# Kernel tuning notes

Measured on AMD Instinct MI355X. Metric: run time of the kernel, lower is better.

The kernel has to match this reference:

```python
import jax, jax.numpy as jnp
import numpy as np

DECAY = 0.999
EPS = 1e-05
COMMIT = 0.25


def _layer_norm(x, g, b, eps=1e-5):
    mu = x.mean(-1, keepdims=True)
    var = ((x - mu) ** 2).mean(-1, keepdims=True)
    return (x - mu) * jax.lax.rsqrt(var + eps) * g + b


def setup_inputs() -> dict:
    key = jax.random.key(0)
    ks = jax.random.split(key, 8)
    B, T, D, M, H = 8, 4096, 512, 1024, 512
    init_bound = 1.0 / 512
    embedding = jax.random.uniform(ks[0], (M, D), jnp.float32, -init_bound, init_bound)
    return {
        "dense_x": jax.random.normal(ks[1], (B, T, D), jnp.float32),
        "dense_padding_mask": jax.random.randint(ks[2], (B, T), 0, 2).astype(bool),
        "labels": jax.random.randint(ks[3], (B, T), 0, M),
        "embedding": embedding,
        "ema_count": jnp.zeros((M,), jnp.float32),
        "ema_weight": embedding,
        "ln1_g": jnp.ones((D,), jnp.float32),
        "ln1_b": jnp.zeros((D,), jnp.float32),
        "W1": jax.random.normal(ks[4], (D, H), jnp.float32) * (1.0 / np.sqrt(D)),
        "ln2_g": jnp.ones((H,), jnp.float32),
        "ln2_b": jnp.zeros((H,), jnp.float32),
        "W2": jax.random.normal(ks[5], (H, M), jnp.float32) * (1.0 / np.sqrt(H)),
    }


def reference(dense_x, dense_padding_mask, labels, embedding, ema_count, ema_weight,
              ln1_g, ln1_b, W1, ln2_g, ln2_b, W2):
    B, T, D = dense_x.shape
    M = embedding.shape[0]
    N = B * T

    # ---- VQ codebook (EMA) ----
    x_flat = jax.lax.stop_gradient(dense_x).reshape(N, D)
    distances = (jnp.sum(embedding ** 2, axis=1)[None, :]
                 + jnp.sum(x_flat ** 2, axis=1, keepdims=True)
                 - 2.0 * (x_flat @ embedding.T))
    indices = jnp.argmin(distances, axis=-1)  # [N]
    quantized = embedding[indices].reshape(B, T, D)

    # EMA codebook update (training path); encodings.sum(0) and encodings.T @ x
    # expressed as scatter-adds instead of materializing [N, M] one-hot.
    counts = jnp.zeros((M,), dense_x.dtype).at[indices].add(1.0)
    new_count = DECAY * ema_count + (1.0 - DECAY) * counts
    n = jnp.sum(new_count)
    new_count = (new_count + EPS) / (n + M * EPS) * n
    dw = jnp.zeros((M, D), dense_x.dtype).at[indices].add(x_flat)
    new_weight = DECAY * ema_weight + (1.0 - DECAY) * dw
    new_embedding = new_weight / new_count[:, None]

    e_latent_loss = (dense_x - jax.lax.stop_gradient(quantized)) ** 2  # [B,T,D]
    vq_loss = COMMIT * e_latent_loss
    quantized_st = dense_x + jax.lax.stop_gradient(quantized - dense_x)

    avg_probs = counts / N
    perplexity = jnp.exp(-jnp.sum(avg_probs * jnp.log(avg_probs + 1e-10)))

    # ---- decoder: LN -> ReLU -> Linear -> LN -> ReLU -> Linear ----
    h = jax.nn.relu(_layer_norm(dense_x, ln1_g, ln1_b)) @ W1      # [B,T,H]
    logits = jax.nn.relu(_layer_norm(h, ln2_g, ln2_b)) @ W2       # [B,T,M]

    # ---- cross-entropy with ignore_index=-1 (padding) ----
    lab = jnp.where(dense_padding_mask, -1, labels)
    valid = lab >= 0
    safe = jnp.where(valid, lab, 0)
    logp = jax.nn.log_softmax(logits, axis=-1)
    ce = -jnp.take_along_axis(logp, safe[..., None], axis=-1)[..., 0]
    recon_loss = jnp.where(valid, ce, 0.0)

    loss = recon_loss + vq_loss.sum(-1)  # [B,T]
    return quantized_st, loss, perplexity, new_embedding, new_count, new_weight
```

## Files before the change

### kernel.cpp

```cpp
#include <hip/hip_runtime.h>


#define N_TOK 32768
#define WAITV(n) __builtin_amdgcn_s_waitcnt(0x0F70 | (n))
#define BAR() __builtin_amdgcn_s_barrier()

typedef __attribute__((ext_vector_type(8))) short short8;
typedef _Float16 half8 __attribute__((ext_vector_type(8)));
typedef __attribute__((ext_vector_type(4))) float f32x4;

__device__ __forceinline__ f32x4 mfma16(short8 a, short8 b, f32x4 c) {
    return __builtin_amdgcn_mfma_f32_16x16x32_bf16(a, b, c, 0, 0, 0);
}
__device__ __forceinline__ f32x4 mfma16h(half8 a, half8 b, f32x4 c) {
    return __builtin_amdgcn_mfma_f32_16x16x32_f16(a, b, c, 0, 0, 0);
}

__device__ __forceinline__ void gl_lds16(const unsigned short* g, char* l) {
    __builtin_amdgcn_global_load_lds(
        (const __attribute__((address_space(1))) void*)g,
        (__attribute__((address_space(3))) void*)l, 16, 0, 0);
}

__device__ __forceinline__ unsigned short f2bf(float x) {
    unsigned u = __float_as_uint(x);
    u += 0x7fffu + ((u >> 16) & 1u);
    return (unsigned short)(u >> 16);
}
__device__ __forceinline__ float bf2f(unsigned short h) {
    return __uint_as_float(((unsigned)h) << 16);
}
__device__ __forceinline__ unsigned short f2h(float x) {
    union { _Float16 h; unsigned short u; } c;
    c.h = (_Float16)x;
    return c.u;
}
__device__ __forceinline__ float h2f(unsigned short u) {
    union { _Float16 h; unsigned short u; } c;
    c.u = u;
    return (float)c.h;
}

__device__ __forceinline__ float waveSum(float v) {
#pragma unroll
    for (int off = 32; off > 0; off >>= 1) v += __shfl_down(v, off, 64);
    return v;
}
__device__ __forceinline__ float xorSum(float v) {
#pragma unroll
    for (int off = 1; off < 64; off <<= 1) v += __shfl_xor(v, off);
    return v;
}

__global__ __launch_bounds__(256) void prep_x_kernel(
        const float* __restrict__ X, const float* __restrict__ g,
        const float* __restrict__ b, unsigned short* __restrict__ Xf,
        unsigned short* __restrict__ A1, unsigned long long* __restrict__ minpack) {
    int tid = threadIdx.x;
    if (tid < 4) minpack[(blockIdx.x << 2) + tid] = ~0ULL;
    int lane = tid & 63;
    int n = (blockIdx.x << 2) + (tid >> 6);
    const float* row = X + ((size_t)n << 9);
    float v[8]; float s = 0.f, ss = 0.f;
#pragma unroll
    for (int i = 0; i < 8; ++i) { v[i] = row[lane + (i << 6)]; s += v[i]; ss += v[i] * v[i]; }
    s = xorSum(s); ss = xorSum(ss);
    float mu = s * (1.f / 512.f);
    float rs = rsqrtf(ss * (1.f / 512.f) - mu * mu + 1e-5f);
#pragma unroll
    for (int i = 0; i < 8; ++i) {
        int c = lane + (i << 6);
        size_t o = ((size_t)n << 9) + c;
        float x = v[i];
        Xf[o] = f2h(x);
        float a = fmaxf((x - mu) * rs * g[c] + b[c], 0.f);
        A1[o] = f2bf(a);
    }
}

__global__ __launch_bounds__(256) void prep_e_kernel(
        const float* __restrict__ E, unsigned short* __restrict__ Ehf,
        unsigned short* __restrict__ Elf, float* __restrict__ e_sq,
        int* __restrict__ izero) {
    if (blockIdx.x < 8) izero[(blockIdx.x << 8) + threadIdx.x] = 0;
    int lane = threadIdx.x & 63;
    int m = (blockIdx.x << 2) + (threadIdx.x >> 6);
    const float* row = E + ((size_t)m << 9);
    float ss = 0.f;
#pragma unroll
    for (int i = 0; i < 8; ++i) {
        int c = lane + (i << 6);
        float x = row[c];
        ss += x * x;
        float xs = x * 512.f;
        unsigned short h = f2h(xs);
        size_t o = ((size_t)m << 9) + c;
        Ehf[o] = h;
        Elf[o] = f2h(xs - h2f(h));
    }
    ss = xorSum(ss);
    if (lane == 0) e_sq[m] = ss * 512.f;
}

__global__ __launch_bounds__(256) void prep_wt_kernel(
        const float* __restrict__ W1, const float* __restrict__ W2,
        unsigned short* __restrict__ W1T, unsigned short* __restrict__ W2T) {
    __shared__ float t[32][33];
    int bx = blockIdx.x;
    const float* W = (bx < 16) ? W1 : W2;
    unsigned short* WT = (bx < 16) ? W1T : W2T;
    int Nw = (bx < 16) ? 512 : 1024;
    int n0 = ((bx < 16) ? bx : (bx - 16)) << 5, k0 = blockIdx.y << 5;
    int tx = threadIdx.x & 31, ty = threadIdx.x >> 5;
#pragma unroll
    for (int l = 0; l < 4; ++l)
        t[ty + (l << 3)][tx] = W[(size_t)(k0 + ty + (l << 3)) * Nw + n0 + tx];
    __syncthreads();
#pragma unroll
    for (int l = 0; l < 4; ++l)
        WT[(((size_t)(n0 + ty + (l << 3))) << 9) + k0 + tx] = f2bf(t[tx][ty + (l << 3)]);
}

__device__ __forceinline__ unsigned long long packDist(float d, int m) {
    unsigned u = __float_as_uint(d);
    u = (u & 0x80000000u) ? ~u : (u | 0x80000000u);
    return ((unsigned long long)u << 32) | (unsigned)m;
}

__device__ __forceinline__ void dist_body(
        int q, int x, char* LB,
        const unsigned short* __restrict__ Xf,
        const unsigned short* __restrict__ Ehf, const unsigned short* __restrict__ Elf,
        const float* __restrict__ e_sq, unsigned long long* __restrict__ minpack) {
    int tid = threadIdx.x, lane = tid & 63, w = tid >> 6;
    int quad = lane >> 4, lanelo = lane & 15;
    int wm = w >> 1, wn = w & 1;
    int row0 = (((q >> 3) << 3) | x) << 8;
    int m0 = (q & 7) << 7;

    int mA = tid & 255, kA = tid >> 8;
    int nB = tid & 127, kB = tid >> 7;
    const unsigned short* pA = Xf  + (((size_t)(row0 + mA)) << 9) + (kA << 3);
    const unsigned short* pH = Ehf + (((size_t)(m0  + nB)) << 9) + (kB << 3);
    const unsigned short* pL = Elf + (((size_t)(m0  + nB)) << 9) + (kB << 3);
    char* dA = LB + (tid << 4);
    char* dB = LB + 16384 + (tid << 4);
    const char* ra  = LB + (quad << 12) + (((wm << 6) + lanelo) << 4);
    const char* rbh = LB + 16384 + (quad << 11) + (((wn << 6) + lanelo) << 4);

    f32x4 acc[4][4];
#pragma unroll
    for (int i = 0; i < 4; ++i)
#pragma unroll
        for (int j = 0; j < 4; ++j) acc[i][j] = 0.f;

    gl_lds16(pA, dA);   gl_lds16(pA + 16, dA + 8192);
    gl_lds16(pH, dB);   gl_lds16(pL, dB + 8192);

#pragma unroll
    for (int it = 0; it < 16; ++it) {
        const int cb = it & 1;
        if (it < 15) {
            const unsigned short* sA = pA + ((it + 1) << 5);
            const unsigned short* sH = pH + ((it + 1) << 5);
            const unsigned short* sL = pL + ((it + 1) << 5);
            char* eA = dA + (cb ^ 1) * 32768;
            char* eB = dB + (cb ^ 1) * 32768;
            gl_lds16(sA, eA);   gl_lds16(sA + 16, eA + 8192);
            gl_lds16(sH, eB);   gl_lds16(sL, eB + 8192);
            WAITV(4);
        } else {
            WAITV(0);
        }
        BAR();
        const char* A  = ra  + cb * 32768;
        const char* Bh = rbh + cb * 32768;
        half8 av[4], bh[4], bl[4];
#pragma unroll
        for (int i = 0; i < 4; ++i) av[i] = *(const half8*)(A + (i << 8));
#pragma unroll
        for (int j = 0; j < 4; ++j) {
            bh[j] = *(const half8*)(Bh + (j << 8));
            bl[j] = *(const half8*)(Bh + 8192 + (j << 8));
        }
#pragma unroll
        for (int i = 0; i < 4; ++i)
#pragma unroll
            for (int j = 0; j < 4; ++j) acc[i][j] = mfma16h(av[i], bh[j], acc[i][j]);
#pragma unroll
        for (int i = 0; i < 4; ++i)
#pragma unroll
            for (int j = 0; j < 4; ++j) acc[i][j] = mfma16h(av[i], bl[j], acc[i][j]);
        BAR();
    }

    float esq[4];
#pragma unroll
    for (int j = 0; j < 4; ++j) esq[j] = e_sq[m0 + (wn << 6) + (j << 4) + lanelo];
#pragma unroll
    for (int i = 0; i < 4; ++i)
#pragma unroll
        for (int r = 0; r < 4; ++r) {
            unsigned long long best = ~0ULL;
#pragma unroll
            for (int j = 0; j < 4; ++j) {
                int code = m0 + (wn << 6) + (j << 4) + lanelo;
                float d = esq[j] - 2.f * acc[i][j][r];
                unsigned long long p = packDist(d, code);
                if (p < best) best = p;
            }
#pragma unroll
            for (int off = 1; off < 16; off <<= 1) {
                unsigned long long q2 = __shfl_xor(best, off);
                if (q2 < best) best = q2;
            }
            if (lanelo == 0) {
                int t = row0 + (wm << 6) + (i << 4) + (quad << 2) + r;
                atomicMin(&minpack[t], best);
            }
        }
}

__device__ __forceinline__ void gemm_core512(
        char* LB, const unsigned short* pA, const unsigned short* pB,
        f32x4 (*acc)[4]) {
    int tid = threadIdx.x, lane = tid & 63, w = tid >> 6;
    int quad = lane >> 4, lanelo = lane & 15;
    int wm = w >> 1, wn = w & 1;
    char* dA = LB + (tid << 4);
    char* dB = LB + 16384 + (tid << 4);
    const char* ra = LB + (quad << 12) + (((wm << 6) + lanelo) << 4);
    const char* rb = LB + 16384 + (quad << 11) + (((wn << 6) + lanelo) << 4);

    gl_lds16(pA, dA);   gl_lds16(pA + 16, dA + 8192);
    gl_lds16(pB, dB);

#pragma unroll
    for (int it = 0; it < 16; ++it) {
        const int cb = it & 1;
        if (it < 15) {
            const unsigned short* sA = pA + ((it + 1) << 5);
            const unsigned short* sB = pB + ((it + 1) << 5);
            char* eA = dA + (cb ^ 1) * 24576;
            char* eB = dB + (cb ^ 1) * 24576;
            gl_lds16(sA, eA);   gl_lds16(sA + 16, eA + 8192);
            gl_lds16(sB, eB);
            WAITV(3);
        } else {
            WAITV(0);
        }
        BAR();
        const char* A = ra + cb * 24576;
        const char* B = rb + cb * 24576;
        short8 af[4], bf4[4];
#pragma unroll
        for (int i = 0; i < 4; ++i) af[i] = *(const short8*)(A + (i << 8));
#pragma unroll
        for (int j = 0; j < 4; ++j) bf4[j] = *(const short8*)(B + (j << 8));
#pragma unroll
        for (int i = 0; i < 4; ++i)
#pragma unroll
            for (int j = 0; j < 4; ++j) acc[i][j] = mfma16(af[i], bf4[j], acc[i][j]);
        BAR();
    }
}

__device__ __forceinline__ void gemm1_body(
        int g, int x, char* LB,
        const unsigned short* __restrict__ A1, const unsigned short* __restrict__ W1T,
        unsigned short* __restrict__ Hb) {
    int tid = threadIdx.x, lane = tid & 63, w = tid >> 6;
    int quad = lane >> 4, lanelo = lane & 15;
    int wm = w >> 1, wn = w & 1;
    int row0 = (((g >> 2) << 3) | x) << 8;
    int n0 = (g & 3) << 7;

    int mA = tid & 255, kA = tid >> 8;
    int nB = tid & 127, kB = tid >> 7;
    const unsigned short* pA = A1  + (((size_t)(row0 + mA)) << 9) + (kA << 3);
    const unsigned short* pB = W1T + (((size_t)(n0   + nB)) << 9) + (kB << 3);

    f32x4 acc[4][4];
#pragma unroll
    for (int i = 0; i < 4; ++i)
#pragma unroll
        for (int j = 0; j < 4; ++j) acc[i][j] = 0.f;

    gemm_core512(LB, pA, pB, acc);

#pragma unroll
    for (int i = 0; i < 4; ++i)
#pragma unroll
        for (int j = 0; j < 4; ++j)
#pragma unroll
            for (int r = 0; r < 4; ++r) {
                int row = row0 + (wm << 6) + (i << 4) + (quad << 2) + r;
                int col = n0 + (wn << 6) + (j << 4) + lanelo;
                Hb[((size_t)row << 9) + col] = f2bf(acc[i][j][r]);
            }
}

__global__ __launch_bounds__(512) void fused1_kernel(
        const unsigned short* __restrict__ Xf,
        const unsigned short* __restrict__ Ehf, const unsigned short* __restrict__ Elf,
        const float* __restrict__ e_sq, unsigned long long* __restrict__ minpack,
        const unsigned short* __restrict__ A1, const unsigned short* __restrict__ W1T,
        unsigned short* __restrict__ Hb) {
    __shared__ __align__(16) char LB[65536];
    int b = blockIdx.x, x = b & 7, m = b >> 3;
    int t = m % 3, g = m / 3;
    if (t < 2) dist_body((g << 1) + t, x, LB, Xf, Ehf, Elf, e_sq, minpack);
    else       gemm1_body(g, x, LB, A1, W1T, Hb);
}

__global__ __launch_bounds__(256) void fused2_kernel(
        const float* __restrict__ X, const float* __restrict__ E,
        const unsigned long long* __restrict__ minpack,
        float* __restrict__ out_q, int* __restrict__ icounts,
        float* __restrict__ vqsum,
        const unsigned short* __restrict__ Hb, const float* __restrict__ g2,
        const float* __restrict__ b2, unsigned short* __restrict__ A2) {
    int nb = blockIdx.x >> 1;
    int lane = threadIdx.x & 63;
    int n = (nb << 2) + (threadIdx.x >> 6);
    if ((blockIdx.x & 1) == 0) {
        int idx = (int)(minpack[n] & 0xFFFFFFFFULL);
        if (lane == 0) atomicAdd(&icounts[idx], 1);
        const float* xr = X + ((size_t)n << 9);
        const float* er = E + ((size_t)idx << 9);
        float s = 0.f;
#pragma unroll
        for (int i = 0; i < 8; ++i) {
            int c = lane + (i << 6);
            float xv = xr[c], q = er[c];
            out_q[((size_t)n << 9) + c] = q;
            float dlt = xv - q;
            s += dlt * dlt;
        }
        s = waveSum(s);
        if (lane == 0) vqsum[n] = 0.25f * s;
    } else {
        const unsigned short* row = Hb + ((size_t)n << 9);
        float v[8]; float s = 0.f, ss = 0.f;
#pragma unroll
        for (int i = 0; i < 8; ++i) { v[i] = bf2f(row[lane + (i << 6)]); s += v[i]; ss += v[i] * v[i]; }
        s = xorSum(s); ss = xorSum(ss);
        float mu = s * (1.f / 512.f);
        float rs = rsqrtf(ss * (1.f / 512.f) - mu * mu + 1e-5f);
#pragma unroll
        for (int i = 0; i < 8; ++i) {
            int c = lane + (i << 6);
            float a = fmaxf((v[i] - mu) * rs * g2[c] + b2[c], 0.f);
            A2[((size_t)n << 9) + c] = f2bf(a);
        }
    }
}

__global__ __launch_bounds__(1024) void codebook_kernel(
        const float* __restrict__ ema_count, const int* __restrict__ icounts,
        float* __restrict__ out_perp, float* __restrict__ out_newcount,
        int* __restrict__ offsets) {
    __shared__ int sc[1024];
    __shared__ float red[16];
    int tid = threadIdx.x;
    int lane = tid & 63, wid = tid >> 6;
    int ic = icounts[tid];
    sc[tid] = ic;
    for (int off = 1; off < 1024; off <<= 1) {
        __syncthreads();
        int v = (tid >= off) ? sc[tid - off] : 0;
        __syncthreads();
        sc[tid] += v;
    }
    offsets[tid] = sc[tid] - ic;
    __syncthreads();

    float cnt = (float)ic;
    float raw = 0.999f * ema_count[tid] + 0.001f * cnt;
    float v = waveSum(raw);
    if (lane == 0) red[wid] = v;
    __syncthreads();
    float nsum = 0.f;
#pragma unroll
    for (int i = 0; i < 16; ++i) nsum += red[i];
    __syncthreads();
    float p = cnt * (1.f / 32768.f);
    float e = p * logf(p + 1e-10f);
    e = waveSum(e);
    if (lane == 0) red[wid] = e;
    __syncthreads();
    float ent = 0.f;
#pragma unroll
    for (int i = 0; i < 16; ++i) ent += red[i];
    float nc = (raw + 1e-5f) / (nsum + 1024.f * 1e-5f) * nsum;
    out_newcount[tid] = nc;
    if (tid == 0) out_perp[0] = expf(-ent);
}

__global__ __launch_bounds__(256) void scatter_kernel(
        const unsigned long long* __restrict__ minpack,
        const int* __restrict__ offsets, int* __restrict__ cursor,
        int* __restrict__ bucket) {
    int n = (blockIdx.x << 8) + threadIdx.x;
    int idx = (int)(minpack[n] & 0xFFFFFFFFULL);
    int pos = atomicAdd(&cursor[idx], 1);
    bucket[offsets[idx] + pos] = n;
}

__device__ __forceinline__ void dw_body(
        int m, char* LB, const float* __restrict__ X,
        const int* __restrict__ bucket, const int* __restrict__ icounts,
        const int* __restrict__ offsets, float* __restrict__ dw) {
    float* comb = (float*)LB;
    int tid = threadIdx.x, lane = tid & 63, w = tid >> 6;
    int cnt = icounts[m], base = offsets[m];
    float acc[8] = {};
    for (int i = w; i < cnt; i += 8) {
        int t = bucket[base + i];
        const float* xr = X + ((size_t)t << 9);
#pragma unroll
        for (int j = 0; j < 8; ++j) acc[j] += xr[lane + (j << 6)];
    }
#pragma unroll
    for (int j = 0; j < 8; ++j) comb[(w << 9) + lane + (j << 6)] = acc[j];
    __syncthreads();
    int c = tid;
    if (c < 512) {
        float s = 0.f;
#pragma unroll
        for (int p = 0; p < 8; ++p) s += comb[(p << 9) + c];
        dw[((size_t)m << 9) + c] = s;
    }
}

__device__ __forceinline__ void gemm2_body(
        int q, int x, char* LB,
        float (*lmax)[2][64], float (*lsum)[2][64], float* llab, int* slab,
        const unsigned short* __restrict__ A2, const unsigned short* __restrict__ W2T,
        const int* __restrict__ mask, const int* __restrict__ labels,
        float* __restrict__ ws_cmax, float* __restrict__ ws_csum,
        float* __restrict__ ws_lab) {
    int tid = threadIdx.x, lane = tid & 63, w = tid >> 6;
    int quad = lane >> 4, lanelo = lane & 15;
    int wm = w >> 1, wn = w & 1;
    int row0 = (((q >> 3) << 3) | x) << 8;
    int cy = q & 7;
    int c0 = cy << 7;
    if (tid < 256) {
        int mk = mask[row0 + tid];
        slab[tid] = mk ? 0 : labels[row0 + tid];
    }
    __syncthreads();

    int mA = tid & 255, kA = tid >> 8;
    int nB = tid & 127, kB = tid >> 7;
    const unsigned short* pA = A2  + (((size_t)(row0 + mA)) << 9) + (kA << 3);
    const unsigned short* pB = W2T + (((size_t)(c0   + nB)) << 9) + (kB << 3);

    f32x4 acc[4][4];
#pragma unroll
    for (int i = 0; i < 4; ++i)
#pragma unroll
        for (int j = 0; j < 4; ++j) acc[i][j] = 0.f;

    gemm_core512(LB, pA, pB, acc);

#pragma unroll
    for (int i = 0; i < 4; ++i)
#pragma unroll
        for (int j = 0; j < 4; ++j)
#pragma unroll
            for (int r = 0; r < 4; ++r) {
                int code = c0 + (wn << 6) + (j << 4) + lanelo;
                int tt = (wm << 6) + (i << 4) + (quad << 2) + r;
                if (code == slab[tt]) llab[tt] = acc[i][j][r];
            }
#pragma unroll
    for (int i = 0; i < 4; ++i)
#pragma unroll
        for (int r = 0; r < 4; ++r) {
            float mx = fmaxf(fmaxf(acc[i][0][r], acc[i][1][r]),
                             fmaxf(acc[i][2][r], acc[i][3][r]));
#pragma unroll
            for (int off = 1; off < 16; off <<= 1) mx = fmaxf(mx, __shfl_xor(mx, off));
            if (lanelo == 0) lmax[wm][wn][(i << 4) + (quad << 2) + r] = mx;
        }
    __syncthreads();
#pragma unroll
    for (int i = 0; i < 4; ++i)
#pragma unroll
        for (int r = 0; r < 4; ++r) {
            int tl = (i << 4) + (quad << 2) + r;
            float cm = fmaxf(lmax[wm][0][tl], lmax[wm][1][tl]);
            float s2 = expf(acc[i][0][r] - cm) + expf(acc[i][1][r] - cm) +
                       expf(acc[i][2][r] - cm) + expf(acc[i][3][r] - cm);
#pragma unroll
            for (int off = 1; off < 16; off <<= 1) s2 += __shfl_xor(s2, off);
            if (lanelo == 0) lsum[wm][wn][tl] = s2;
        }
    __syncthreads();
    if (tid < 256) {
        int wmi = tid >> 6, tl = tid & 63;
        int token = row0 + tid;
        float cm = fmaxf(lmax[wmi][0][tl], lmax[wmi][1][tl]);
        float cs = lsum[wmi][0][tl] + lsum[wmi][1][tl];
        size_t o = ((size_t)cy << 15) + token;
        ws_cmax[o] = cm;
        ws_csum[o] = cs;
        if ((slab[tid] >> 7) == cy) ws_lab[token] = llab[tid];
    }
}

__global__ __launch_bounds__(512) void fused3_kernel(
        const unsigned short* __restrict__ A2, const unsigned short* __restrict__ W2T,
        const int* __restrict__ mask, const int* __restrict__ labels,
        float* __restrict__ ws_cmax, float* __restrict__ ws_csum,
        float* __restrict__ ws_lab,
        const float* __restrict__ X, const int* __restrict__ bucket,
        const int* __restrict__ icounts, const int* __restrict__ offsets,
        float* __restrict__ dw) {
    __shared__ __align__(16) char LB[49152];
    __shared__ float lmax[4][2][64], lsum[4][2][64], llab[256];
    __shared__ int slab[256];
    int b = blockIdx.x, x = b & 7, m = b >> 3;
    int t = m & 1, g = m >> 1;
    if (t == 0) gemm2_body(g, x, LB, lmax, lsum, llab, slab,
                           A2, W2T, mask, labels, ws_cmax, ws_csum, ws_lab);
    else        dw_body((g << 3) | x, LB, X, bucket, icounts, offsets, dw);
}

__global__ __launch_bounds__(256) void epilogue_kernel(
        const float* __restrict__ ema_weight, const float* __restrict__ dw,
        const float* __restrict__ newcount, float* __restrict__ out_neww,
        float* __restrict__ out_newemb,
        const float* __restrict__ ws_cmax, const float* __restrict__ ws_csum,
        const float* __restrict__ ws_lab, const int* __restrict__ mask,
        const float* __restrict__ vqsum, float* __restrict__ loss_out) {
    int bx = blockIdx.x;
    if (bx < 2048) {
        int i = (bx << 8) + threadIdx.x;
        float nw = 0.999f * ema_weight[i] + 0.001f * dw[i];
        out_neww[i] = nw;
        out_newemb[i] = nw / newcount[i >> 9];
    } else {
        int n = ((bx - 2048) << 8) + threadIdx.x;
        float m[8], s[8];
#pragma unroll
        for (int c = 0; c < 8; ++c) {
            m[c] = ws_cmax[(c << 15) + n];
            s[c] = ws_csum[(c << 15) + n];
        }
        float gm = m[0];
#pragma unroll
        for (int c = 1; c < 8; ++c) gm = fmaxf(gm, m[c]);
        float se = 0.f;
#pragma unroll
        for (int c = 0; c < 8; ++c) se += s[c] * expf(m[c] - gm);
        float ce = -(ws_lab[n] - gm - logf(se));
        loss_out[n] = (mask[n] ? 0.f : ce) + vqsum[n];
    }
}

extern "C" void kernel_launch(void* const* d_in, const int* in_sizes, int n_in,
                              void* d_out, int out_size, void* d_ws, size_t ws_size,
                              hipStream_t stream) {
    const float* X          = (const float*)d_in[0];
    const int*   mask       = (const int*)d_in[1];
    const int*   labels     = (const int*)d_in[2];
    const float* E          = (const float*)d_in[3];
    const float* ema_count  = (const float*)d_in[4];
    const float* ema_weight = (const float*)d_in[5];
    const float* g1 = (const float*)d_in[6];
    const float* b1 = (const float*)d_in[7];
    const float* W1 = (const float*)d_in[8];
    const float* g2 = (const float*)d_in[9];
    const float* b2 = (const float*)d_in[10];
    const float* W2 = (const float*)d_in[11];

    float* out = (float*)d_out;
    float* out_q        = out;
    float* out_loss     = out + 16777216;
    float* out_perp     = out + 16809984;
    float* out_newemb   = out + 16809985;
    float* out_newcount = out + 17334273;
    float* out_neww     = out + 17335297;

    float* w = (float*)d_ws;
    float* vqsum = w;  w += 32768;
    float* e_sq = w;   w += 1024;
    float* dwbuf = w;  w += 524288;
    unsigned long long* minpack = (unsigned long long*)w; w += 65536;
    float* ws_cmax = w; w += 262144;
    float* ws_csum = w; w += 262144;
    float* ws_lab  = w; w += 32768;
    int* icounts = (int*)w; w += 1024;
    int* cursor  = (int*)w; w += 1024;
    int* offsets = (int*)w; w += 1024;
    int* bucket  = (int*)w; w += 32768;
    unsigned short* Ehf = (unsigned short*)w; w += 262144;
    unsigned short* Elf = (unsigned short*)w; w += 262144;
    unsigned short* W1T = (unsigned short*)w; w += 131072;
    unsigned short* W2T = (unsigned short*)w; w += 262144;
    unsigned short* Xf  = (unsigned short*)w; w += 8388608;
    unsigned short* A1  = (unsigned short*)w; w += 8388608;
    unsigned short* Hb  = (unsigned short*)w; w += 8388608;
    unsigned short* A2  = Xf;

    prep_e_kernel<<<256, 256, 0, stream>>>(E, Ehf, Elf, e_sq, icounts);
    prep_wt_kernel<<<dim3(48, 16), 256, 0, stream>>>(W1, W2, W1T, W2T);
    prep_x_kernel<<<8192, 256, 0, stream>>>(X, g1, b1, Xf, A1, minpack);
    fused1_kernel<<<1536, 512, 0, stream>>>(Xf, Ehf, Elf, e_sq, minpack,
                                            A1, W1T, Hb);
    fused2_kernel<<<16384, 256, 0, stream>>>(X, E, minpack, out_q, icounts,
                                             vqsum, Hb, g2, b2, A2);
    codebook_kernel<<<1, 1024, 0, stream>>>(ema_count, icounts, out_perp,
                                            out_newcount, offsets);
    scatter_kernel<<<128, 256, 0, stream>>>(minpack, offsets, cursor, bucket);
    fused3_kernel<<<2048, 512, 0, stream>>>(A2, W2T, mask, labels,
                                            ws_cmax, ws_csum, ws_lab,
                                            X, bucket, icounts, offsets, dwbuf);
    epilogue_kernel<<<2176, 256, 0, stream>>>(ema_weight, dwbuf, out_newcount,
                                              out_neww, out_newemb,
                                              ws_cmax, ws_csum, ws_lab,
                                              mask, vqsum, out_loss);
}
```

Before: 486.7 us.

## Split fused GEMM2/dw kernel into separate dw and smaller-tile GEMM2 kernels

Breaks the fused kernel, which interleaved GEMM2 blocks and codebook dw-accumulation blocks, into two launches. dw_kernel uses 256-thread blocks, one per code. GEMM2 becomes a 256-thread kernel with 128x128 tiles and an inline double-buffered global-to-LDS pipeline over K in steps of 64, replacing the shared 512-thread gemm_core512. The aim is better occupancy and load balance, since dw blocks with skewed counts no longer share a grid with the GEMM tiles. The cost is an extra launch and more A re-reads from the smaller row tiles.

```diff
diff --git a/kernel.cpp b/kernel.cpp
--- a/kernel.cpp
+++ b/kernel.cpp
@@ -407,55 +407,56 @@
     bucket[offsets[idx] + pos] = n;
 }
 
-__device__ __forceinline__ void dw_body(
-        int m, char* LB, const float* __restrict__ X,
-        const int* __restrict__ bucket, const int* __restrict__ icounts,
-        const int* __restrict__ offsets, float* __restrict__ dw) {
-    float* comb = (float*)LB;
+__global__ __launch_bounds__(256) void dw_kernel(
+        const float* __restrict__ X, const int* __restrict__ bucket,
+        const int* __restrict__ icounts, const int* __restrict__ offsets,
+        float* __restrict__ dw) {
+    __shared__ float comb[4][512];
     int tid = threadIdx.x, lane = tid & 63, w = tid >> 6;
+    int m = blockIdx.x;
     int cnt = icounts[m], base = offsets[m];
     float acc[8] = {};
-    for (int i = w; i < cnt; i += 8) {
+    for (int i = w; i < cnt; i += 4) {
         int t = bucket[base + i];
         const float* xr = X + ((size_t)t << 9);
 #pragma unroll
         for (int j = 0; j < 8; ++j) acc[j] += xr[lane + (j << 6)];
     }
 #pragma unroll
-    for (int j = 0; j < 8; ++j) comb[(w << 9) + lane + (j << 6)] = acc[j];
-    __syncthreads();
-    int c = tid;
-    if (c < 512) {
-        float s = 0.f;
-#pragma unroll
-        for (int p = 0; p < 8; ++p) s += comb[(p << 9) + c];
-        dw[((size_t)m << 9) + c] = s;
-    }
-}
-
-__device__ __forceinline__ void gemm2_body(
-        int q, int x, char* LB,
-        float (*lmax)[2][64], float (*lsum)[2][64], float* llab, int* slab,
+    for (int j = 0; j < 8; ++j) comb[w][lane + (j << 6)] = acc[j];
+    __syncthreads();
+    for (int c = tid; c < 512; c += 256)
+        dw[((size_t)m << 9) + c] = comb[0][c] + comb[1][c] + comb[2][c] + comb[3][c];
+}
+
+__global__ __launch_bounds__(256) void gemm2_chunk_kernel(
         const unsigned short* __restrict__ A2, const unsigned short* __restrict__ W2T,
         const int* __restrict__ mask, const int* __restrict__ labels,
         float* __restrict__ ws_cmax, float* __restrict__ ws_csum,
         float* __restrict__ ws_lab) {
+    __shared__ __align__(16) short L[2][2][8192];
+    __shared__ float lmax[2][2][64], lsum[2][2][64], llab[128];
+    __shared__ int slab[128];
     int tid = threadIdx.x, lane = tid & 63, w = tid >> 6;
     int quad = lane >> 4, lanelo = lane & 15;
     int wm = w >> 1, wn = w & 1;
-    int row0 = (((q >> 3) << 3) | x) << 8;
-    int cy = q & 7;
+    int bid = blockIdx.x, xcd = bid & 7, s = bid >> 3;
+    int row0 = (((s >> 3) << 3) | xcd) << 7;
+    int cy = s & 7;
     int c0 = cy << 7;
-    if (tid < 256) {
+    if (tid < 128) {
         int mk = mask[row0 + tid];
         slab[tid] = mk ? 0 : labels[row0 + tid];
     }
     __syncthreads();
 
-    int mA = tid & 255, kA = tid >> 8;
-    int nB = tid & 127, kB = tid >> 7;
-    const unsigned short* pA = A2  + (((size_t)(row0 + mA)) << 9) + (kA << 3);
-    const unsigned short* pB = W2T + (((size_t)(c0   + nB)) << 9) + (kB << 3);
+    int srow = ((w & 1) << 6) + lane;
+    int skoff = (w >> 1) << 5;
+    const unsigned short* pA = A2  + (((size_t)(row0 + srow)) << 9) + skoff;
+    const unsigned short* pB = W2T + (((size_t)(c0   + srow)) << 9) + skoff;
+    char* ldsB = (char*)&L[0][0][0] + ((w >> 1) << 13) + ((w & 1) << 10) + (lane << 4);
+    const char* ra = (const char*)&L[0][0][0] + (quad << 11) + (((wm << 6) + lanelo) << 4);
+    const char* rb = (const char*)&L[0][0][0] + 16384 + (quad << 11) + (((wn << 6) + lanelo) << 4);
 
     f32x4 acc[4][4];
 #pragma unroll
@@ -463,7 +464,43 @@
 #pragma unroll
         for (int j = 0; j < 4; ++j) acc[i][j] = 0.f;
 
-    gemm_core512(LB, pA, pB, acc);
+    gl_lds16(pA, ldsB);           gl_lds16(pA + 8, ldsB + 2048);
+    gl_lds16(pA + 16, ldsB + 4096); gl_lds16(pA + 24, ldsB + 6144);
+    gl_lds16(pB, ldsB + 16384);   gl_lds16(pB + 8, ldsB + 18432);
+    gl_lds16(pB + 16, ldsB + 20480); gl_lds16(pB + 24, ldsB + 22528);
+
+#pragma unroll
+    for (int it = 0; it < 8; ++it) {
+        const int cb = it & 1;
+        if (it < 7) {
+            const unsigned short* sA = pA + ((it + 1) << 6);
+            const unsigned short* sB = pB + ((it + 1) << 6);
+            char* d = ldsB + (cb ^ 1) * 32768;
+            gl_lds16(sA, d);           gl_lds16(sA + 8, d + 2048);
+            gl_lds16(sA + 16, d + 4096); gl_lds16(sA + 24, d + 6144);
+            gl_lds16(sB, d + 16384);   gl_lds16(sB + 8, d + 18432);
+            gl_lds16(sB + 16, d + 20480); gl_lds16(sB + 24, d + 22528);
+            WAITV(8);
+        } else {
+            WAITV(0);
+        }
+        BAR();
+        const char* A = ra + cb * 32768;
+        const char* B = rb + cb * 32768;
+#pragma unroll
+        for (int kk = 0; kk < 2; ++kk) {
+            short8 af[4], bf4[4];
+#pragma unroll
+            for (int i = 0; i < 4; ++i) af[i] = *(const short8*)(A + (kk << 13) + (i << 8));
+#pragma unroll
+            for (int j = 0; j < 4; ++j) bf4[j] = *(const short8*)(B + (kk << 13) + (j << 8));
+#pragma unroll
+            for (int i = 0; i < 4; ++i)
+#pragma unroll
+                for (int j = 0; j < 4; ++j) acc[i][j] = mfma16(af[i], bf4[j], acc[i][j]);
+        }
+        BAR();
+    }
 
 #pragma unroll
     for (int i = 0; i < 4; ++i)
@@ -499,7 +536,7 @@
             if (lanelo == 0) lsum[wm][wn][tl] = s2;
         }
     __syncthreads();
-    if (tid < 256) {
+    if (tid < 128) {
         int wmi = tid >> 6, tl = tid & 63;
         int token = row0 + tid;
         float cm = fmaxf(lmax[wmi][0][tl], lmax[wmi][1][tl]);
@@ -509,24 +546,6 @@
         ws_csum[o] = cs;
         if ((slab[tid] >> 7) == cy) ws_lab[token] = llab[tid];
     }
-}
-
-__global__ __launch_bounds__(512) void fused3_kernel(
-        const unsigned short* __restrict__ A2, const unsigned short* __restrict__ W2T,
-        const int* __restrict__ mask, const int* __restrict__ labels,
-        float* __restrict__ ws_cmax, float* __restrict__ ws_csum,
-        float* __restrict__ ws_lab,
-        const float* __restrict__ X, const int* __restrict__ bucket,
-        const int* __restrict__ icounts, const int* __restrict__ offsets,
-        float* __restrict__ dw) {
-    __shared__ __align__(16) char LB[49152];
-    __shared__ float lmax[4][2][64], lsum[4][2][64], llab[256];
-    __shared__ int slab[256];
-    int b = blockIdx.x, x = b & 7, m = b >> 3;
-    int t = m & 1, g = m >> 1;
-    if (t == 0) gemm2_body(g, x, LB, lmax, lsum, llab, slab,
-                           A2, W2T, mask, labels, ws_cmax, ws_csum, ws_lab);
-    else        dw_body((g << 3) | x, LB, X, bucket, icounts, offsets, dw);
 }
 
 __global__ __launch_bounds__(256) void epilogue_kernel(
@@ -616,9 +635,9 @@
     codebook_kernel<<<1, 1024, 0, stream>>>(ema_count, icounts, out_perp,
                                             out_newcount, offsets);
     scatter_kernel<<<128, 256, 0, stream>>>(minpack, offsets, cursor, bucket);
-    fused3_kernel<<<2048, 512, 0, stream>>>(A2, W2T, mask, labels,
-                                            ws_cmax, ws_csum, ws_lab,
-                                            X, bucket, icounts, offsets, dwbuf);
+    dw_kernel<<<1024, 256, 0, stream>>>(X, bucket, icounts, offsets, dwbuf);
+    gemm2_chunk_kernel<<<2048, 256, 0, stream>>>(A2, W2T, mask, labels,
+                                                 ws_cmax, ws_csum, ws_lab);
     epilogue_kernel<<<2176, 256, 0, stream>>>(ema_weight, dwbuf, out_newcount,
                                               out_neww, out_newemb,
                                               ws_cmax, ws_csum, ws_lab,
```

Measured after the change: 469.4 us. 1.04x faster.
